# Performance work log

Hardware: AMD Instinct MI355X
Metric: run time of the kernel (lower is better)

The kernel has to match this reference:

```python
import jax, jax.numpy as jnp
import numpy as np

ALPHA_LO = float(np.exp(-1.0 / 5.0))   # 0.8187
ALPHA_HI = float(np.exp(-1.0 / 25.0))  # 0.9608
BN_EPS = 1e-5

B, T, D_IN, H = 32, 2000, 512, 512


def setup_inputs() -> dict:
    key = jax.random.key(0)
    ks = jax.random.split(key, 5)
    x = jax.random.normal(ks[0], (B, T, D_IN), dtype=jnp.float32)
    W = jax.random.normal(ks[1], (H, D_IN), dtype=jnp.float32) / np.sqrt(D_IN)
    b = jax.random.normal(ks[2], (H,), dtype=jnp.float32) * 0.01
    alpha = jax.random.uniform(ks[3], (H,), dtype=jnp.float32,
                               minval=ALPHA_LO, maxval=ALPHA_HI)
    gamma = jnp.ones((H,), dtype=jnp.float32)
    beta = jnp.zeros((H,), dtype=jnp.float32)
    ut0 = jax.random.uniform(ks[4], (B, H), dtype=jnp.float32)
    return {"x": x, "W": W, "b": b, "alpha": alpha,
            "gamma": gamma, "beta": beta, "ut0": ut0}


def reference(x, W, b, alpha, gamma, beta, ut0):
    # Linear: [B,T,Din] @ [Din,H] + b
    Wx = jnp.einsum("btd,hd->bth", x, W) + b
    # BatchNorm1d (training forward): stats over flattened (B*T) dim
    flat = Wx.reshape(-1, Wx.shape[-1])
    mean = flat.mean(axis=0)
    var = flat.var(axis=0)  # biased, as torch BN uses for normalization
    Wx = ((flat - mean) * jax.lax.rsqrt(var + BN_EPS) * gamma + beta).reshape(Wx.shape)
    # Readout cell: leaky integration + softmax accumulation over time
    a = jnp.clip(alpha, ALPHA_LO, ALPHA_HI)

    def step(carry, wxt):
        ut, acc = carry
        ut = a * ut + (1.0 - a) * wxt          # [B,H]
        acc = acc + jax.nn.softmax(ut, axis=1)
        return (ut, acc), None

    wx_t = jnp.transpose(Wx, (1, 0, 2))  # [T,B,H]
    (_, out), _ = jax.lax.scan(step, (ut0, jnp.zeros_like(ut0)), wx_t)
    return out[:, None, :]  # [B,1,H]
```

## Files before the change

### kernel.cpp

```cpp
#include <hip/hip_runtime.h>
#include <hip/hip_bf16.h>
#include <stdint.h>


namespace {
constexpr int kB = 32;
constexpr int kT = 2000;
constexpr int kD = 512;
constexpr int kH = 512;
constexpr int kM = kB * kT;
constexpr int kL = 20;
constexpr int kC = kT / kL;
constexpr float kALo = 0.81873075307798182f;
constexpr float kAHi = 0.96078943915232320f;

typedef __bf16 bf16x8 __attribute__((ext_vector_type(8)));
typedef float floatx16 __attribute__((ext_vector_type(16)));

__device__ __forceinline__ float bf2f(unsigned short u) {
  return __builtin_bit_cast(float, (unsigned)u << 16);
}
__device__ __forceinline__ float clipa(float a) {
  return fminf(fmaxf(a, kALo), kAHi);
}
__device__ __forceinline__ float pow20(float a) {
  const float a2 = a * a, a4 = a2 * a2, a5 = a4 * a;
  const float a10 = a5 * a5;
  return a10 * a10;
}
__device__ __forceinline__ void gld_lds16(const void* g, void* l) {
  __builtin_amdgcn_global_load_lds(
      (const __attribute__((address_space(1))) uint32_t*)g,
      (__attribute__((address_space(3))) uint32_t*)(uintptr_t)l, 16, 0, 0);
}

__global__ __launch_bounds__(256) void wcvt_k(const float* __restrict__ W,
                                              __bf16* __restrict__ Wbf) {
  const int t = blockIdx.x * 256 + threadIdx.x;
  const float4 a0 = ((const float4*)W)[t * 2];
  const float4 a1 = ((const float4*)W)[t * 2 + 1];
  bf16x8 v;
  v[0] = (__bf16)a0.x; v[1] = (__bf16)a0.y; v[2] = (__bf16)a0.z; v[3] = (__bf16)a0.w;
  v[4] = (__bf16)a1.x; v[5] = (__bf16)a1.y; v[6] = (__bf16)a1.z; v[7] = (__bf16)a1.w;
  *(bf16x8*)(Wbf + (size_t)t * 8) = v;
}

__global__ __launch_bounds__(512, 2) void gemm_k(const float* __restrict__ X,
                                                 const __bf16* __restrict__ Wbf,
                                                 unsigned short* __restrict__ Wxb,
                                                 float* __restrict__ partial) {
  __shared__ __align__(16) char AsB[2][4 * 1024];
  __shared__ __align__(16) char BsB[2][32 * 1024];
  __shared__ float sred[2][kH];
  const int tid = threadIdx.x;
  const size_t row0 = (size_t)blockIdx.x * 64;
  const int w = tid >> 6, L = tid & 63;
  const int rt = w >> 2, ct0 = (w & 3) * 4;
  const int lhalf = L >> 5, l32 = L & 31;
  const int am = tid >> 2, akq = tid & 3;
  const int a_off = ((am >> 5) * 2 + (akq >> 1)) * 1024 + ((akq & 1) * 32 + (am & 31)) * 16;
  const float* xptr = X + (row0 + am) * kD + akq * 8;

  floatx16 acc[4] = {};
  float4 ap0, ap1;

  auto loadA = [&](int s) {
    if (tid < 256) {
      const float4* p = (const float4*)(xptr + s * 32);
      ap0 = p[0]; ap1 = p[1];
    }
  };
  auto storeA = [&](int buf) {
    if (tid < 256) {
      bf16x8 v;
      v[0] = (__bf16)ap0.x; v[1] = (__bf16)ap0.y; v[2] = (__bf16)ap0.z; v[3] = (__bf16)ap0.w;
      v[4] = (__bf16)ap1.x; v[5] = (__bf16)ap1.y; v[6] = (__bf16)ap1.z; v[7] = (__bf16)ap1.w;
      *(bf16x8*)(AsB[buf] + a_off) = v;
    }
  };
  auto dmaB = [&](int s, int buf) {
#pragma unroll
    for (int j = 0; j < 4; ++j) {
      const int q = w * 4 + j;
      const int n = (q >> 1) * 32 + l32;
      const int k = s * 32 + (q & 1) * 16 + lhalf * 8;
      gld_lds16(Wbf + (size_t)n * kD + k, BsB[buf] + q * 1024);
    }
  };

  loadA(0);
  dmaB(0, 0);
  storeA(0);
  __syncthreads();

#pragma unroll 1
  for (int s = 0; s < 16; ++s) {
    const int cur = s & 1, nxt = cur ^ 1;
    if (s < 15) {
      dmaB(s + 1, nxt);
      loadA(s + 1);
    }
#pragma unroll
    for (int kh = 0; kh < 2; ++kh) {
      const bf16x8 af = *(const bf16x8*)(AsB[cur] + (rt * 2 + kh) * 1024 + L * 16);
#pragma unroll
      for (int c = 0; c < 4; ++c) {
        const bf16x8 bfr =
            *(const bf16x8*)(BsB[cur] + ((ct0 + c) * 2 + kh) * 1024 + L * 16);
        acc[c] = __builtin_amdgcn_mfma_f32_32x32x16_bf16(af, bfr, acc[c], 0, 0, 0);
      }
    }
    if (s < 15) storeA(nxt);
    __syncthreads();
  }

  sred[0][tid] = 0.f;
  sred[1][tid] = 0.f;
  __syncthreads();
#pragma unroll
  for (int c = 0; c < 4; ++c) {
    float s = 0.f, q = 0.f;
#pragma unroll
    for (int r = 0; r < 16; ++r) {
      const float v = acc[c][r];
      s += v;
      q += v * v;
    }
    s += __shfl_xor(s, 32);
    q += __shfl_xor(q, 32);
    if (lhalf == 0) {
      atomicAdd(&sred[0][(ct0 + c) * 32 + l32], s);
      atomicAdd(&sred[1][(ct0 + c) * 32 + l32], q);
    }
  }
#pragma unroll
  for (int c = 0; c < 4; ++c) {
    const int col = (ct0 + c) * 32 + l32;
#pragma unroll
    for (int r = 0; r < 16; ++r) {
      const int row = rt * 32 + 4 * lhalf + (r & 3) + 8 * (r >> 2);
      const unsigned short u = __builtin_bit_cast(unsigned short, (__bf16)acc[c][r]);
      const unsigned un = __shfl_down((unsigned)u, 1);
      if ((l32 & 1) == 0)
        *(unsigned*)(Wxb + (row0 + row) * (size_t)kH + col) = (unsigned)u | (un << 16);
    }
  }
  __syncthreads();
  partial[(size_t)blockIdx.x * 1024 + tid] = sred[0][tid];
  partial[(size_t)blockIdx.x * 1024 + 512 + tid] = sred[1][tid];
}

__global__ __launch_bounds__(512) void red1_k(const float* __restrict__ partial,
                                              float* __restrict__ partial2) {
  const int tid = threadIdx.x;
  const int r0 = blockIdx.x * 25;
  float s0 = 0.f, s1 = 0.f;
#pragma unroll 5
  for (int r = 0; r < 25; ++r) {
    s0 += partial[(size_t)(r0 + r) * 1024 + tid];
    s1 += partial[(size_t)(r0 + r) * 1024 + 512 + tid];
  }
  partial2[(size_t)blockIdx.x * 1024 + tid] = s0;
  partial2[(size_t)blockIdx.x * 1024 + 512 + tid] = s1;
}

__global__ __launch_bounds__(512) void finalize_k(const float* __restrict__ partial2,
                                                  const float* __restrict__ alpha,
                                                  const float* __restrict__ gamma,
                                                  const float* __restrict__ beta,
                                                  float* __restrict__ prm) {
  const int h = threadIdx.x;
  float s0 = 0.f, s1 = 0.f;
#pragma unroll 8
  for (int r = 0; r < 40; ++r) {
    s0 += partial2[(size_t)r * 1024 + h];
    s1 += partial2[(size_t)r * 1024 + 512 + h];
  }
  const float inv_n = 1.0f / (float)kM;
  const float mean = s0 * inv_n;
  const float var = s1 * inv_n - mean * mean;
  const float sc = gamma[h] * rsqrtf(var + 1e-5f);
  const float sh = beta[h] - mean * sc;
  const float a = clipa(alpha[h]);
  prm[h] = sc;
  prm[kH + h] = sh;
  prm[2 * kH + h] = a;
  prm[3 * kH + h] = 1.0f - a;
  prm[4 * kH + h] = pow20(a);
}

__global__ __launch_bounds__(256) void agg_k(const unsigned short* __restrict__ Wxb,
                                             const float* __restrict__ alpha,
                                             float* __restrict__ vbuf) {
  const int g = blockIdx.x;
  const int b = g / (kC / 4), cg = g % (kC / 4);
  const int wv = threadIdx.x >> 6, lane = threadIdx.x & 63;
  const int c = cg * 4 + wv;
  const int h0 = lane * 8;
  float a[8], v[8];
  const float4 av0 = *(const float4*)(alpha + h0);
  const float4 av1 = *(const float4*)(alpha + h0 + 4);
  a[0] = av0.x; a[1] = av0.y; a[2] = av0.z; a[3] = av0.w;
  a[4] = av1.x; a[5] = av1.y; a[6] = av1.z; a[7] = av1.w;
#pragma unroll
  for (int j = 0; j < 8; ++j) { a[j] = clipa(a[j]); v[j] = 0.f; }
  const unsigned short* base = Wxb + ((size_t)b * kT + (size_t)c * kL) * kH + h0;
#pragma unroll
  for (int i = 0; i < kL; ++i) {
    const uint4 p = *(const uint4*)(base + (size_t)i * kH);
    const unsigned pw[4] = {p.x, p.y, p.z, p.w};
#pragma unroll
    for (int d = 0; d < 4; ++d) {
      const float w0 = bf2f((unsigned short)(pw[d] & 0xffff));
      const float w1 = bf2f((unsigned short)(pw[d] >> 16));
      v[2 * d] = a[2 * d] * v[2 * d] + (1.f - a[2 * d]) * w0;
      v[2 * d + 1] = a[2 * d + 1] * v[2 * d + 1] + (1.f - a[2 * d + 1]) * w1;
    }
  }
  float* dst = vbuf + ((size_t)b * kC + c) * kH + h0;
  *(float4*)dst = make_float4(v[0], v[1], v[2], v[3]);
  *(float4*)(dst + 4) = make_float4(v[4], v[5], v[6], v[7]);
}

__global__ __launch_bounds__(512) void scan_k(const float* __restrict__ ut0,
                                              const float* __restrict__ alpha,
                                              const float* __restrict__ prm,
                                              float* __restrict__ vbuf) {
  const int b = blockIdx.x;
  const int h = threadIdx.x;
  const float a20 = pow20(clipa(alpha[h]));
  const float sc = prm[h];
  const float shc = prm[kH + h] * (1.0f - a20);
  float u = ut0[(size_t)b * kH + h];
  float vc[10];
#pragma unroll 1
  for (int cb = 0; cb < kC; cb += 10) {
#pragma unroll
    for (int j = 0; j < 10; ++j)
      vc[j] = vbuf[((size_t)b * kC + cb + j) * kH + h];
#pragma unroll
    for (int j = 0; j < 10; ++j) {
      vbuf[((size_t)b * kC + cb + j) * kH + h] = u;
      u = a20 * u + sc * vc[j] + shc;
    }
  }
}

__global__ __launch_bounds__(128) void soft_k(const unsigned short* __restrict__ Wxb,
                                              const float* __restrict__ prm,
                                              const float* __restrict__ ustart,
                                              float* __restrict__ accp) {
  __shared__ float part[kL][2];
  __shared__ float zinv[kL];
  const int bc = blockIdx.x;
  const int b = bc / kC, c = bc % kC;
  const int t = threadIdx.x;
  const int wv = t >> 6, lane = t & 63;
  const int h0 = t * 4;
  const float4 sc = *(const float4*)(prm + h0);
  const float4 sh = *(const float4*)(prm + kH + h0);
  const float4 aa = *(const float4*)(prm + 2 * kH + h0);
  const float4 om = *(const float4*)(prm + 3 * kH + h0);
  float4 u = *(const float4*)(ustart + (size_t)bc * kH + h0);
  const unsigned short* base = Wxb + ((size_t)b * kT + (size_t)c * kL) * kH + h0;
  float e[kL][4];
#pragma unroll
  for (int i = 0; i < kL; ++i) {
    const uint2 p = *(const uint2*)(base + (size_t)i * kH);
    const float w0 = bf2f((unsigned short)(p.x & 0xffff)) * sc.x + sh.x;
    const float w1 = bf2f((unsigned short)(p.x >> 16)) * sc.y + sh.y;
    const float w2 = bf2f((unsigned short)(p.y & 0xffff)) * sc.z + sh.z;
    const float w3 = bf2f((unsigned short)(p.y >> 16)) * sc.w + sh.w;
    u.x = aa.x * u.x + om.x * w0;
    u.y = aa.y * u.y + om.y * w1;
    u.z = aa.z * u.z + om.z * w2;
    u.w = aa.w * u.w + om.w * w3;
    e[i][0] = __expf(u.x); e[i][1] = __expf(u.y);
    e[i][2] = __expf(u.z); e[i][3] = __expf(u.w);
    float s = (e[i][0] + e[i][1]) + (e[i][2] + e[i][3]);
#pragma unroll
    for (int off = 32; off > 0; off >>= 1) s += __shfl_xor(s, off);
    if (lane == 0) part[i][wv] = s;
  }
  __syncthreads();
  if (t < kL) zinv[t] = 1.0f / (part[t][0] + part[t][1]);
  __syncthreads();
  float4 o = make_float4(0.f, 0.f, 0.f, 0.f);
#pragma unroll
  for (int i = 0; i < kL; ++i) {
    const float z = zinv[i];
    o.x += e[i][0] * z; o.y += e[i][1] * z;
    o.z += e[i][2] * z; o.w += e[i][3] * z;
  }
  *(float4*)(accp + (size_t)bc * kH + h0) = o;
}

__global__ __launch_bounds__(128) void out_red_k(const float* __restrict__ accp,
                                                 float* __restrict__ out) {
  const int b = blockIdx.x >> 2, q = blockIdx.x & 3;
  const int h = q * 128 + threadIdx.x;
  float s = 0.f;
#pragma unroll 5
  for (int c = 0; c < kC; ++c) s += accp[((size_t)b * kC + c) * kH + h];
  out[(size_t)b * kH + h] = s;
}

}

extern "C" void kernel_launch(void* const* d_in, const int* in_sizes, int n_in,
                              void* d_out, int out_size, void* d_ws, size_t ws_size,
                              hipStream_t stream) {
  const float* x = (const float*)d_in[0];
  const float* Wm = (const float*)d_in[1];
  const float* alpha = (const float*)d_in[3];
  const float* gamma = (const float*)d_in[4];
  const float* beta = (const float*)d_in[5];
  const float* ut0 = (const float*)d_in[6];
  float* out = (float*)d_out;

  float* wsp = (float*)d_ws;
  float* vbuf = wsp;
  float* accp = vbuf + (size_t)kB * kC * kH;
  float* partial = accp + (size_t)kB * kC * kH;
  float* partial2 = partial + (size_t)1000 * 1024;
  float* prm = partial2 + (size_t)40 * 1024;
  __bf16* Wbf = (__bf16*)(prm + 5 * kH);
  unsigned short* Wxb = (unsigned short*)(Wbf + (size_t)kH * kD);

  wcvt_k<<<128, 256, 0, stream>>>(Wm, Wbf);
  gemm_k<<<kM / 64, 512, 0, stream>>>(x, Wbf, Wxb, partial);
  red1_k<<<40, 512, 0, stream>>>(partial, partial2);
  agg_k<<<kB * (kC / 4), 256, 0, stream>>>(Wxb, alpha, vbuf);
  finalize_k<<<1, 512, 0, stream>>>(partial2, alpha, gamma, beta, prm);
  scan_k<<<kB, 512, 0, stream>>>(ut0, alpha, prm, vbuf);
  soft_k<<<kB * kC, 128, 0, stream>>>(Wxb, prm, vbuf, accp);
  out_red_k<<<kB * 4, 128, 0, stream>>>(accp, out);
}
```

Before: 336.9 us.

## Fuse chunk aggregation into GEMM epilogue and switch B tile to register-staged padded LDS

The separate agg_k pass over Wxb is removed. Its per-chunk leaky-integration sums are now built in the GEMM epilogue from the accumulators, weighted by alpha powers. Blocks whose 64 rows straddle a chunk boundary write partial sums into two planes, and the scan adds those planes. The GEMM also drops global_load_lds DMA double buffering for register-staged single-buffered padded LDS, and raises the occupancy hint to 4. The aim is to save one full read of the bf16 intermediate. The cost is extra epilogue math, an added memset, and possibly a less overlapped main loop.

```diff
diff --git a/kernel.cpp b/kernel.cpp
--- a/kernel.cpp
+++ b/kernel.cpp
@@ -11,8 +11,10 @@
 constexpr int kM = kB * kT;
 constexpr int kL = 20;
 constexpr int kC = kT / kL;
+constexpr int kNC = kB * kC;
 constexpr float kALo = 0.81873075307798182f;
 constexpr float kAHi = 0.96078943915232320f;
+constexpr int kPad = 40;
 
 typedef __bf16 bf16x8 __attribute__((ext_vector_type(8)));
 typedef float floatx16 __attribute__((ext_vector_type(16)));
@@ -27,11 +29,6 @@
   const float a2 = a * a, a4 = a2 * a2, a5 = a4 * a;
   const float a10 = a5 * a5;
   return a10 * a10;
-}
-__device__ __forceinline__ void gld_lds16(const void* g, void* l) {
-  __builtin_amdgcn_global_load_lds(
-      (const __attribute__((address_space(1))) uint32_t*)g,
-      (__attribute__((address_space(3))) uint32_t*)(uintptr_t)l, 16, 0, 0);
 }
 
 __global__ __launch_bounds__(256) void wcvt_k(const float* __restrict__ W,
@@ -45,86 +42,85 @@
   *(bf16x8*)(Wbf + (size_t)t * 8) = v;
 }
 
-__global__ __launch_bounds__(512, 2) void gemm_k(const float* __restrict__ X,
+__global__ __launch_bounds__(512, 4) void gemm_k(const float* __restrict__ X,
                                                  const __bf16* __restrict__ Wbf,
+                                                 const float* __restrict__ alpha,
                                                  unsigned short* __restrict__ Wxb,
-                                                 float* __restrict__ partial) {
-  __shared__ __align__(16) char AsB[2][4 * 1024];
-  __shared__ __align__(16) char BsB[2][32 * 1024];
+                                                 float* __restrict__ partial,
+                                                 float* __restrict__ vplanes) {
+  __shared__ __align__(16) __bf16 As[64][kPad];
+  __shared__ __align__(16) __bf16 Bs[512][kPad];
   __shared__ float sred[2][kH];
+  float* aggLds = (float*)&Bs[0][0];
+
   const int tid = threadIdx.x;
-  const size_t row0 = (size_t)blockIdx.x * 64;
+  const int r0i = blockIdx.x * 64;
+  const size_t row0 = (size_t)r0i;
   const int w = tid >> 6, L = tid & 63;
   const int rt = w >> 2, ct0 = (w & 3) * 4;
   const int lhalf = L >> 5, l32 = L & 31;
   const int am = tid >> 2, akq = tid & 3;
-  const int a_off = ((am >> 5) * 2 + (akq >> 1)) * 1024 + ((akq & 1) * 32 + (am & 31)) * 16;
-  const float* xptr = X + (row0 + am) * kD + akq * 8;
+  const int bn = tid >> 2, bkq = tid & 3;
 
   floatx16 acc[4] = {};
   float4 ap0, ap1;
+  uint4 br[4];
 
   auto loadA = [&](int s) {
     if (tid < 256) {
-      const float4* p = (const float4*)(xptr + s * 32);
+      const float4* p = (const float4*)(X + (row0 + am) * kD + s * 32 + akq * 8);
       ap0 = p[0]; ap1 = p[1];
     }
   };
-  auto storeA = [&](int buf) {
+  auto loadB = [&](int s) {
+#pragma unroll
+    for (int j = 0; j < 4; ++j)
+      br[j] = *(const uint4*)(Wbf + (size_t)(bn + 128 * j) * kD + s * 32 + bkq * 8);
+  };
+  auto storeLds = [&]() {
     if (tid < 256) {
       bf16x8 v;
       v[0] = (__bf16)ap0.x; v[1] = (__bf16)ap0.y; v[2] = (__bf16)ap0.z; v[3] = (__bf16)ap0.w;
       v[4] = (__bf16)ap1.x; v[5] = (__bf16)ap1.y; v[6] = (__bf16)ap1.z; v[7] = (__bf16)ap1.w;
-      *(bf16x8*)(AsB[buf] + a_off) = v;
-    }
+      *(bf16x8*)&As[am][akq * 8] = v;
+    }
+#pragma unroll
+    for (int j = 0; j < 4; ++j)
+      *(uint4*)&Bs[bn + 128 * j][bkq * 8] = br[j];
   };
-  auto dmaB = [&](int s, int buf) {
-#pragma unroll
-    for (int j = 0; j < 4; ++j) {
-      const int q = w * 4 + j;
-      const int n = (q >> 1) * 32 + l32;
-      const int k = s * 32 + (q & 1) * 16 + lhalf * 8;
-      gld_lds16(Wbf + (size_t)n * kD + k, BsB[buf] + q * 1024);
-    }
-  };
 
   loadA(0);
-  dmaB(0, 0);
-  storeA(0);
-  __syncthreads();
-
+  loadB(0);
 #pragma unroll 1
   for (int s = 0; s < 16; ++s) {
-    const int cur = s & 1, nxt = cur ^ 1;
-    if (s < 15) {
-      dmaB(s + 1, nxt);
-      loadA(s + 1);
-    }
+    storeLds();
+    __syncthreads();
+    if (s < 15) { loadA(s + 1); loadB(s + 1); }
 #pragma unroll
     for (int kh = 0; kh < 2; ++kh) {
-      const bf16x8 af = *(const bf16x8*)(AsB[cur] + (rt * 2 + kh) * 1024 + L * 16);
+      const bf16x8 af = *(const bf16x8*)&As[rt * 32 + l32][kh * 16 + lhalf * 8];
 #pragma unroll
       for (int c = 0; c < 4; ++c) {
-        const bf16x8 bfr =
-            *(const bf16x8*)(BsB[cur] + ((ct0 + c) * 2 + kh) * 1024 + L * 16);
+        const bf16x8 bfr = *(const bf16x8*)&Bs[(ct0 + c) * 32 + l32][kh * 16 + lhalf * 8];
         acc[c] = __builtin_amdgcn_mfma_f32_32x32x16_bf16(af, bfr, acc[c], 0, 0, 0);
       }
     }
-    if (s < 15) storeA(nxt);
     __syncthreads();
   }
 
   sred[0][tid] = 0.f;
   sred[1][tid] = 0.f;
+  aggLds[tid] = 0.f; aggLds[512 + tid] = 0.f;
+  aggLds[1024 + tid] = 0.f; aggLds[1536 + tid] = 0.f;
   __syncthreads();
+
 #pragma unroll
   for (int c = 0; c < 4; ++c) {
     float s = 0.f, q = 0.f;
 #pragma unroll
     for (int r = 0; r < 16; ++r) {
       const float v = acc[c][r];
-      s += v;
-      q += v * v;
+      s += v; q += v * v;
     }
     s += __shfl_xor(s, 32);
     q += __shfl_xor(q, 32);
@@ -133,6 +129,39 @@
       atomicAdd(&sred[1][(ct0 + c) * 32 + l32], q);
     }
   }
+
+  const int r0m = r0i % 20;
+  const int gc0 = r0i / 20;
+  const int s_base = r0m + rt * 32 + 4 * lhalf;
+#pragma unroll
+  for (int c = 0; c < 4; ++c) {
+    const int h = (ct0 + c) * 32 + l32;
+    const float a = clipa(alpha[h]);
+    const float la = log2f(a);
+    const float oma = 1.0f - a;
+    float q0 = 0.f, q1 = 0.f, q2 = 0.f, q3 = 0.f;
+#pragma unroll
+    for (int r = 0; r < 16; ++r) {
+      const int off = (r & 3) + 8 * (r >> 2);
+      const int sf = s_base + off;
+      const int slot = sf / 20;
+      const int e = 19 + slot * 20 - sf;
+      const float cv = acc[c][r] * oma * exp2f((float)e * la);
+      q0 += (slot == 0) ? cv : 0.f;
+      q1 += (slot == 1) ? cv : 0.f;
+      q2 += (slot == 2) ? cv : 0.f;
+      q3 += (slot == 3) ? cv : 0.f;
+    }
+    q0 += __shfl_xor(q0, 32); q1 += __shfl_xor(q1, 32);
+    q2 += __shfl_xor(q2, 32); q3 += __shfl_xor(q3, 32);
+    if (lhalf == 0) {
+      atomicAdd(&aggLds[h], q0);
+      atomicAdd(&aggLds[512 + h], q1);
+      atomicAdd(&aggLds[1024 + h], q2);
+      atomicAdd(&aggLds[1536 + h], q3);
+    }
+  }
+
 #pragma unroll
   for (int c = 0; c < 4; ++c) {
     const int col = (ct0 + c) * 32 + l32;
@@ -146,6 +175,12 @@
     }
   }
   __syncthreads();
+#pragma unroll
+  for (int s = 0; s < 4; ++s) {
+    const int gcs = gc0 + s;
+    const int pl = (s == 0 && r0m != 0) ? 1 : 0;
+    vplanes[(size_t)pl * kNC * kH + (size_t)gcs * kH + tid] = aggLds[s * 512 + tid];
+  }
   partial[(size_t)blockIdx.x * 1024 + tid] = sred[0][tid];
   partial[(size_t)blockIdx.x * 1024 + 512 + tid] = sred[1][tid];
 }
@@ -189,58 +224,28 @@
   prm[4 * kH + h] = pow20(a);
 }
 
-__global__ __launch_bounds__(256) void agg_k(const unsigned short* __restrict__ Wxb,
-                                             const float* __restrict__ alpha,
-                                             float* __restrict__ vbuf) {
-  const int g = blockIdx.x;
-  const int b = g / (kC / 4), cg = g % (kC / 4);
-  const int wv = threadIdx.x >> 6, lane = threadIdx.x & 63;
-  const int c = cg * 4 + wv;
-  const int h0 = lane * 8;
-  float a[8], v[8];
-  const float4 av0 = *(const float4*)(alpha + h0);
-  const float4 av1 = *(const float4*)(alpha + h0 + 4);
-  a[0] = av0.x; a[1] = av0.y; a[2] = av0.z; a[3] = av0.w;
-  a[4] = av1.x; a[5] = av1.y; a[6] = av1.z; a[7] = av1.w;
-#pragma unroll
-  for (int j = 0; j < 8; ++j) { a[j] = clipa(a[j]); v[j] = 0.f; }
-  const unsigned short* base = Wxb + ((size_t)b * kT + (size_t)c * kL) * kH + h0;
-#pragma unroll
-  for (int i = 0; i < kL; ++i) {
-    const uint4 p = *(const uint4*)(base + (size_t)i * kH);
-    const unsigned pw[4] = {p.x, p.y, p.z, p.w};
-#pragma unroll
-    for (int d = 0; d < 4; ++d) {
-      const float w0 = bf2f((unsigned short)(pw[d] & 0xffff));
-      const float w1 = bf2f((unsigned short)(pw[d] >> 16));
-      v[2 * d] = a[2 * d] * v[2 * d] + (1.f - a[2 * d]) * w0;
-      v[2 * d + 1] = a[2 * d + 1] * v[2 * d + 1] + (1.f - a[2 * d + 1]) * w1;
-    }
-  }
-  float* dst = vbuf + ((size_t)b * kC + c) * kH + h0;
-  *(float4*)dst = make_float4(v[0], v[1], v[2], v[3]);
-  *(float4*)(dst + 4) = make_float4(v[4], v[5], v[6], v[7]);
-}
-
 __global__ __launch_bounds__(512) void scan_k(const float* __restrict__ ut0,
                                               const float* __restrict__ alpha,
                                               const float* __restrict__ prm,
-                                              float* __restrict__ vbuf) {
+                                              float* __restrict__ vplanes) {
   const int b = blockIdx.x;
   const int h = threadIdx.x;
   const float a20 = pow20(clipa(alpha[h]));
   const float sc = prm[h];
   const float shc = prm[kH + h] * (1.0f - a20);
+  const float* p1 = vplanes + (size_t)kNC * kH;
   float u = ut0[(size_t)b * kH + h];
   float vc[10];
 #pragma unroll 1
   for (int cb = 0; cb < kC; cb += 10) {
 #pragma unroll
-    for (int j = 0; j < 10; ++j)
-      vc[j] = vbuf[((size_t)b * kC + cb + j) * kH + h];
-#pragma unroll
     for (int j = 0; j < 10; ++j) {
-      vbuf[((size_t)b * kC + cb + j) * kH + h] = u;
+      const size_t idx = ((size_t)b * kC + cb + j) * kH + h;
+      vc[j] = vplanes[idx] + p1[idx];
+    }
+#pragma unroll
+    for (int j = 0; j < 10; ++j) {
+      vplanes[((size_t)b * kC + cb + j) * kH + h] = u;
       u = a20 * u + sc * vc[j] + shc;
     }
   }
@@ -319,20 +324,20 @@
   float* out = (float*)d_out;
 
   float* wsp = (float*)d_ws;
-  float* vbuf = wsp;
-  float* accp = vbuf + (size_t)kB * kC * kH;
-  float* partial = accp + (size_t)kB * kC * kH;
+  float* vplanes = wsp;
+  float* accp = vplanes + (size_t)2 * kNC * kH;
+  float* partial = accp + (size_t)kNC * kH;
   float* partial2 = partial + (size_t)1000 * 1024;
   float* prm = partial2 + (size_t)40 * 1024;
   __bf16* Wbf = (__bf16*)(prm + 5 * kH);
   unsigned short* Wxb = (unsigned short*)(Wbf + (size_t)kH * kD);
 
+  (void)hipMemsetAsync(vplanes + (size_t)kNC * kH, 0, (size_t)kNC * kH * sizeof(float), stream);
   wcvt_k<<<128, 256, 0, stream>>>(Wm, Wbf);
-  gemm_k<<<kM / 64, 512, 0, stream>>>(x, Wbf, Wxb, partial);
+  gemm_k<<<kM / 64, 512, 0, stream>>>(x, Wbf, alpha, Wxb, partial, vplanes);
   red1_k<<<40, 512, 0, stream>>>(partial, partial2);
-  agg_k<<<kB * (kC / 4), 256, 0, stream>>>(Wxb, alpha, vbuf);
   finalize_k<<<1, 512, 0, stream>>>(partial2, alpha, gamma, beta, prm);
-  scan_k<<<kB, 512, 0, stream>>>(ut0, alpha, prm, vbuf);
-  soft_k<<<kB * kC, 128, 0, stream>>>(Wxb, prm, vbuf, accp);
+  scan_k<<<kB, 512, 0, stream>>>(ut0, alpha, prm, vplanes);
+  soft_k<<<kNC, 128, 0, stream>>>(Wxb, prm, vplanes, accp);
   out_red_k<<<kB * 4, 128, 0, stream>>>(accp, out);
 }
```

New measurement: 439.1 us. 30.3% more time.
